# Performance work log

Measured on AMD Instinct MI355X. Metric: run time of the kernel, lower is better.

The kernel has to match this reference:

```python
import jax, jax.numpy as jnp
import numpy as np

BS, X_DIM, KEY_DIM, N_KEYS, TOPK = 16384, 4096, 512, 4096, 16


def setup_inputs() -> dict:
    key = jax.random.key(0)
    k_x, k_keys, k_w, k_b = jax.random.split(key, 4)
    bound = 1.0 / np.sqrt(X_DIM)  # torch Linear default init range
    return {
        "x": jax.random.normal(k_x, (BS, X_DIM), dtype=jnp.float32),
        "keys": jax.random.normal(k_keys, (N_KEYS, KEY_DIM), dtype=jnp.float32),
        "W": jax.random.uniform(k_w, (KEY_DIM, X_DIM), dtype=jnp.float32, minval=-bound, maxval=bound),
        "b": jax.random.uniform(k_b, (KEY_DIM,), dtype=jnp.float32, minval=-bound, maxval=bound),
        "topk": TOPK,
    }


def reference(x, keys, W, b, topk):
    # query = projection(x): [bs, key_dim]
    query = jnp.einsum("bx,kx->bk", x, W) + b
    # scores = query @ keys^T: [bs, n_keys]
    scores = jnp.einsum("bd,nd->bn", query, keys)
    real_topk = min(keys.shape[0], topk)
    topk_scores, topk_idx = jax.lax.top_k(scores, real_topk)  # [bs, k]
    bs = scores.shape[0]
    rows = jnp.arange(bs)[:, None]
    # scatter topk scores into a zero tensor, then softmax over the full row
    gates = jnp.zeros_like(scores).at[rows, topk_idx].set(topk_scores)
    gates = jax.nn.softmax(gates, axis=1)
    return (gates, scores)
```

## Files before the change

### kernel.cpp

```cpp
#include <hip/hip_runtime.h>
#include <stdint.h>

#define BS_T   16384
#define XDIM   4096
#define KDIM   512
#define NKEYS  4096
#define KTOP   16

typedef _Float16 half8  __attribute__((ext_vector_type(8)));
typedef float    floatx4 __attribute__((ext_vector_type(4)));

__device__ static inline void gload_lds16(const void* g, void* l) {
  __builtin_amdgcn_global_load_lds(
      (const __attribute__((address_space(1))) uint32_t*)(uintptr_t)g,
      (__attribute__((address_space(3))) uint32_t*)(uint32_t)(uintptr_t)l,
      16, 0, 0);
}

#define FULL_BAR() do { __builtin_amdgcn_sched_barrier(0); \
                        __builtin_amdgcn_s_barrier(); \
                        __builtin_amdgcn_sched_barrier(0); } while (0)

__global__ __launch_bounds__(256) void cvt_f32_f16_v(const float* __restrict__ in,
                                                     _Float16* __restrict__ out, int n8) {
  int stride = gridDim.x * 256;
  for (int i = blockIdx.x * 256 + threadIdx.x; i < n8; i += stride) {
    float4 v0 = ((const float4*)in)[2 * i];
    float4 v1 = ((const float4*)in)[2 * i + 1];
    half8 h = { (_Float16)v0.x, (_Float16)v0.y, (_Float16)v0.z, (_Float16)v0.w,
                (_Float16)v1.x, (_Float16)v1.y, (_Float16)v1.z, (_Float16)v1.w };
    ((half8*)out)[i] = h;
  }
}

__global__ __launch_bounds__(512, 1)
void gemm1_pipe(const float* __restrict__ X, const _Float16* __restrict__ Wh,
                const float* __restrict__ bias, _Float16* __restrict__ Q) {
  __shared__ __align__(16) _Float16 ldsA[2][64 * 64];
  __shared__ __align__(16) _Float16 ldsB[2][512 * 64];

  const int tid  = threadIdx.x;
  const int lane = tid & 63;
  const int wid  = tid >> 6;
  const int rowBase = blockIdx.x * 64;
  const int wc  = wid * 64;
  const int l15 = lane & 15;
  const int q4  = lane >> 4;
  const int sub   = lane >> 3;
  const int gslot = (lane & 7) ^ sub;

  const int arow  = tid >> 3;
  const int aslot = tid & 7;
  const float* aSrcT = X + (size_t)(rowBase + arow) * XDIM + aslot * 8;
  const int aoff = arow * 128 + ((aslot * 16) ^ ((arow & 7) << 4));
  const _Float16* const bSrc = Wh + (size_t)(wc + sub) * XDIM + gslot * 8;

  auto stageB = [&](int kt, int buf) {
    char* bd = (char*)&ldsB[buf][0] + wid * 8192;
    #pragma unroll
    for (int i = 0; i < 8; ++i)
      gload_lds16(bSrc + (size_t)i * 8 * XDIM + kt, bd + i * 1024);
  };
  auto writeA = [&](int buf, float4 v0, float4 v1) {
    half8 h = { (_Float16)v0.x, (_Float16)v0.y, (_Float16)v0.z, (_Float16)v0.w,
                (_Float16)v1.x, (_Float16)v1.y, (_Float16)v1.z, (_Float16)v1.w };
    *(half8*)((char*)&ldsA[buf][0] + aoff) = h;
  };
  auto ld8 = [&](const char* base, int row, int s) {
    return *(const half8*)(base + row * 128 + ((s * 16) ^ ((row & 7) << 4)));
  };

  floatx4 acc[4][4];
  #pragma unroll
  for (int m = 0; m < 4; ++m)
    #pragma unroll
    for (int n = 0; n < 4; ++n)
      acc[m][n] = (floatx4)0.0f;

  float4 p0  = *(const float4*)(aSrcT);
  float4 p1  = *(const float4*)(aSrcT + 4);
  float4 aw0 = *(const float4*)(aSrcT + 64);
  float4 aw1 = *(const float4*)(aSrcT + 68);
  stageB(0, 0);
  stageB(64, 1);
  writeA(0, p0, p1);
  asm volatile("s_waitcnt lgkmcnt(0)" ::: "memory");
  asm volatile("s_waitcnt vmcnt(8)" ::: "memory");
  FULL_BAR();

  #pragma unroll 2
  for (int t = 0; t < 64; ++t) {
    const int cu = t & 1;
    const char* bA = (const char*)&ldsA[cu][0];
    const char* bB = (const char*)&ldsB[cu][0];

    half8 a[4][2], b[4][2];
    #pragma unroll
    for (int m = 0; m < 4; ++m)
      #pragma unroll
      for (int kk = 0; kk < 2; ++kk)
        a[m][kk] = ld8(bA, m * 16 + l15, kk * 4 + q4);
    #pragma unroll
    for (int n = 0; n < 4; ++n)
      #pragma unroll
      for (int kk = 0; kk < 2; ++kk)
        b[n][kk] = ld8(bB, wc + n * 16 + l15, kk * 4 + q4);
    float4 nl0, nl1;
    if (t < 62) {
      nl0 = *(const float4*)(aSrcT + (t + 2) * 64);
      nl1 = *(const float4*)(aSrcT + (t + 2) * 64 + 4);
    }
    asm volatile("s_waitcnt lgkmcnt(0)" ::: "memory");
    __builtin_amdgcn_sched_barrier(0);
    if (t < 62) stageB((t + 2) * 64, cu);
    __builtin_amdgcn_sched_barrier(0);

    __builtin_amdgcn_s_setprio(1);
    #pragma unroll
    for (int m = 0; m < 4; ++m)
      #pragma unroll
      for (int n = 0; n < 4; ++n)
        #pragma unroll
        for (int kk = 0; kk < 2; ++kk)
          acc[m][n] = __builtin_amdgcn_mfma_f32_16x16x32_f16(a[m][kk], b[n][kk], acc[m][n], 0, 0, 0);
    __builtin_amdgcn_s_setprio(0);

    if (t < 63) writeA(cu ^ 1, aw0, aw1);
    asm volatile("s_waitcnt lgkmcnt(0)" ::: "memory");
    __builtin_amdgcn_sched_barrier(0);
    if (t < 62)       asm volatile("s_waitcnt vmcnt(10)" ::: "memory");
    else if (t == 62) asm volatile("s_waitcnt vmcnt(0)"  ::: "memory");
    FULL_BAR();
    aw0 = nl0; aw1 = nl1;
  }

  #pragma unroll
  for (int m = 0; m < 4; ++m) {
    #pragma unroll
    for (int n = 0; n < 4; ++n) {
      int col = wc + n * 16 + l15;
      float bv = bias[col];
      #pragma unroll
      for (int r = 0; r < 4; ++r) {
        int row = rowBase + m * 16 + q4 * 4 + r;
        Q[(size_t)row * KDIM + col] = (_Float16)(acc[m][n][r] + bv);
      }
    }
  }
}

__global__ __launch_bounds__(512, 2)
void gemm2_pipe(const _Float16* __restrict__ Aq, const _Float16* __restrict__ Bk,
                float* __restrict__ outp) {
  __shared__ __align__(16) _Float16 ldsA[2][256 * 64];
  __shared__ __align__(16) _Float16 ldsB[2][256 * 64];

  const int tid  = threadIdx.x;
  const int lane = tid & 63;
  const int wid  = tid >> 6;
  const int cpx  = gridDim.x >> 3;
  const int bid  = (blockIdx.x & 7) * cpx + (blockIdx.x >> 3);
  const int nCol = NKEYS / 256;
  const int rowBase = (bid / nCol) * 256;
  const int colBase = (bid % nCol) * 256;
  const int wm = wid >> 2;
  const int wn = wid & 3;
  const int l15 = lane & 15;
  const int q4  = lane >> 4;
  const int sub   = lane >> 3;
  const int gslot = (lane & 7) ^ sub;

  const _Float16* aSrc = Aq + (size_t)rowBase * KDIM;
  const _Float16* bSrc = Bk + (size_t)colBase * KDIM;

  auto stageHalf = [&](const _Float16* src, char* ldsbase, int kt, int h) {
    #pragma unroll
    for (int j = 0; j < 2; ++j) {
      int g = h * 16 + wid * 2 + j;
      gload_lds16(src + (size_t)(g * 8 + sub) * KDIM + kt + gslot * 8,
                  ldsbase + g * 1024);
    }
  };
  auto ld8 = [&](const char* base, int row, int s) {
    return *(const half8*)(base + row * 128 + ((s * 16) ^ ((row & 7) << 4)));
  };

  floatx4 acc[8][4];
  #pragma unroll
  for (int m = 0; m < 8; ++m)
    #pragma unroll
    for (int n = 0; n < 4; ++n)
      acc[m][n] = (floatx4)0.0f;

  stageHalf(aSrc, (char*)ldsA[0], 0, 0);
  stageHalf(aSrc, (char*)ldsA[0], 0, 1);
  stageHalf(bSrc, (char*)ldsB[0], 0, 0);
  stageHalf(bSrc, (char*)ldsB[0], 0, 1);
  stageHalf(aSrc, (char*)ldsA[1], 64, 0);
  stageHalf(aSrc, (char*)ldsA[1], 64, 1);
  stageHalf(bSrc, (char*)ldsB[1], 64, 0);
  stageHalf(bSrc, (char*)ldsB[1], 64, 1);
  asm volatile("s_waitcnt vmcnt(8)" ::: "memory");
  FULL_BAR();

  for (int t = 0; t < 8; ++t) {
    const char* bA = (const char*)ldsA[t & 1];
    const char* bB = (const char*)ldsB[t & 1];
    char* sA = (char*)ldsA[t & 1];
    char* sB = (char*)ldsB[t & 1];
    const int ktn = (t + 2) * 64;
    const bool st = (t < 6);

    half8 a[4][2], b[4][2];

    #pragma unroll
    for (int m = 0; m < 4; ++m)
      #pragma unroll
      for (int kk = 0; kk < 2; ++kk)
        a[m][kk] = ld8(bA, wm * 128 + m * 16 + l15, kk * 4 + q4);
    #pragma unroll
    for (int n = 0; n < 4; ++n)
      #pragma unroll
      for (int kk = 0; kk < 2; ++kk)
        b[n][kk] = ld8(bB, wn * 64 + n * 16 + l15, kk * 4 + q4);
    FULL_BAR();
    asm volatile("s_waitcnt lgkmcnt(0)" ::: "memory");
    __builtin_amdgcn_sched_barrier(0);
    __builtin_amdgcn_s_setprio(1);
    #pragma unroll
    for (int m = 0; m < 4; ++m)
      #pragma unroll
      for (int n = 0; n < 2; ++n)
        #pragma unroll
        for (int kk = 0; kk < 2; ++kk)
          acc[m][n] = __builtin_amdgcn_mfma_f32_16x16x32_f16(a[m][kk], b[n][kk], acc[m][n], 0, 0, 0);
    __builtin_amdgcn_s_setprio(0);
    FULL_BAR();

    if (st) stageHalf(bSrc, sB, ktn, 0);
    __builtin_amdgcn_sched_barrier(0);
    __builtin_amdgcn_s_setprio(1);
    #pragma unroll
    for (int m = 0; m < 4; ++m)
      #pragma unroll
      for (int n = 2; n < 4; ++n)
        #pragma unroll
        for (int kk = 0; kk < 2; ++kk)
          acc[m][n] = __builtin_amdgcn_mfma_f32_16x16x32_f16(a[m][kk], b[n][kk], acc[m][n], 0, 0, 0);
    __builtin_amdgcn_s_setprio(0);
    FULL_BAR();

    #pragma unroll
    for (int m = 0; m < 4; ++m)
      #pragma unroll
      for (int kk = 0; kk < 2; ++kk)
        a[m][kk] = ld8(bA, wm * 128 + (m + 4) * 16 + l15, kk * 4 + q4);
    if (st) stageHalf(bSrc, sB, ktn, 1);
    FULL_BAR();
    asm volatile("s_waitcnt lgkmcnt(0)" ::: "memory");
    __builtin_amdgcn_sched_barrier(0);
    __builtin_amdgcn_s_setprio(1);
    #pragma unroll
    for (int m = 0; m < 4; ++m)
      #pragma unroll
      for (int n = 0; n < 2; ++n)
        #pragma unroll
        for (int kk = 0; kk < 2; ++kk)
          acc[m + 4][n] = __builtin_amdgcn_mfma_f32_16x16x32_f16(a[m][kk], b[n][kk], acc[m + 4][n], 0, 0, 0);
    __builtin_amdgcn_s_setprio(0);
    FULL_BAR();

    if (st) { stageHalf(aSrc, sA, ktn, 0); stageHalf(aSrc, sA, ktn, 1); }
    __builtin_amdgcn_sched_barrier(0);
    __builtin_amdgcn_s_setprio(1);
    #pragma unroll
    for (int m = 0; m < 4; ++m)
      #pragma unroll
      for (int n = 2; n < 4; ++n)
        #pragma unroll
        for (int kk = 0; kk < 2; ++kk)
          acc[m + 4][n] = __builtin_amdgcn_mfma_f32_16x16x32_f16(a[m][kk], b[n][kk], acc[m + 4][n], 0, 0, 0);
    __builtin_amdgcn_s_setprio(0);
    __builtin_amdgcn_sched_barrier(0);
    if (t < 6)      asm volatile("s_waitcnt vmcnt(8)" ::: "memory");
    else if (t == 6) asm volatile("s_waitcnt vmcnt(0)" ::: "memory");
    FULL_BAR();
  }

  #pragma unroll
  for (int m = 0; m < 8; ++m) {
    #pragma unroll
    for (int n = 0; n < 4; ++n) {
      int col = colBase + wn * 64 + n * 16 + l15;
      #pragma unroll
      for (int r = 0; r < 4; ++r) {
        int row = rowBase + wm * 128 + m * 16 + q4 * 4 + r;
        outp[(size_t)row * NKEYS + col] = acc[m][n][r];
      }
    }
  }
}

__global__ __launch_bounds__(256) void topk_gates_kernel(const float* __restrict__ scores,
                                                         float* __restrict__ gates) {
  __shared__ uint32_t hist[4096];
  __shared__ uint32_t sA[256];
  __shared__ uint32_t av[16], ai[16];
  __shared__ uint32_t sk[KTOP], si[KTOP];
  __shared__ uint32_t cntA, cntC;
  __shared__ int s_p; __shared__ uint32_t s_above;
  __shared__ float gk[KTOP]; __shared__ float s_gother;

  const int tid  = threadIdx.x;
  const int lane = tid & 63;
  const int w    = tid >> 6;
  const float* srow = scores + (size_t)blockIdx.x * NKEYS;

  uint4 z4 = {0, 0, 0, 0};
  #pragma unroll
  for (int i = 0; i < 4; ++i) ((uint4*)hist)[tid + 256 * i] = z4;
  if (tid == 0) { cntA = 0; cntC = 0; }

  uint32_t key[16];
  const int base = (w << 10) + (lane << 4);
  {
    const float4* p4 = (const float4*)(srow + base);
    #pragma unroll
    for (int i = 0; i < 4; ++i) {
      float4 t = p4[i];
      float tv[4] = { t.x, t.y, t.z, t.w };
      #pragma unroll
      for (int c = 0; c < 4; ++c) {
        uint32_t u = __float_as_uint(tv[c]);
        key[i * 4 + c] = u ^ (uint32_t)(((int32_t)u >> 31) | 0x80000000);
      }
    }
  }
  __syncthreads();

  #pragma unroll
  for (int j = 0; j < 16; ++j) atomicAdd(&hist[key[j] >> 20], 1u);
  __syncthreads();

  uint32_t h[16];
  #pragma unroll
  for (int i = 0; i < 16; ++i) h[i] = hist[tid * 16 + i];
  uint32_t sfx[17]; sfx[16] = 0;
  #pragma unroll
  for (int i = 15; i >= 0; --i) sfx[i] = sfx[i + 1] + h[i];
  sA[tid] = sfx[0];
  __syncthreads();
  uint32_t s = sfx[0];
  #pragma unroll
  for (int off = 1; off < 256; off <<= 1) {
    uint32_t add = (tid + off < 256) ? sA[tid + off] : 0;
    __syncthreads();
    s += add; sA[tid] = s;
    __syncthreads();
  }
  const uint32_t exclHi = s - sfx[0];

  #pragma unroll
  for (int i = 0; i < 16; ++i) {
    uint32_t cg = exclHi + sfx[i + 1];
    if (cg < KTOP && cg + h[i] >= KTOP) { s_p = tid * 16 + i; s_above = cg; }
  }
  __syncthreads();
  const uint32_t p = (uint32_t)s_p;
  const uint32_t above = s_above;
  const uint32_t need = KTOP - above;

  uint32_t* ck = hist;
  uint32_t* ci = hist + 2048;
  #pragma unroll
  for (int j = 0; j < 16; ++j) {
    uint32_t b = key[j] >> 20;
    if (b >= p) {
      uint32_t idx = (uint32_t)(base + j);
      if (b > p) { uint32_t pos = atomicAdd(&cntA, 1u); av[pos] = key[j]; ai[pos] = idx; }
      else       { uint32_t pos = atomicAdd(&cntC, 1u); if (pos < 2048u) { ck[pos] = key[j]; ci[pos] = idx; } }
    }
  }
  __syncthreads();

  const uint32_t nA = cntA;
  if (tid < nA) { sk[tid] = av[tid]; si[tid] = ai[tid]; }

  if (w == 0) {
    const uint32_t nC = min(cntC, 2048u);
    for (uint32_t k = 0; k < need; ++k) {
      uint32_t bk = 0, bi = 0xFFFFFFFFu, bp = 0;
      for (uint32_t c = lane; c < nC; c += 64) {
        uint32_t kk = ck[c], ii = ci[c];
        if (kk > bk || (kk == bk && ii < bi)) { bk = kk; bi = ii; bp = c; }
      }
      #pragma unroll
      for (int off = 32; off >= 1; off >>= 1) {
        uint32_t ok = __shfl_down(bk, off);
        uint32_t oi = __shfl_down(bi, off);
        uint32_t op = __shfl_down(bp, off);
        if (ok > bk || (ok == bk && oi < bi)) { bk = ok; bi = oi; bp = op; }
      }
      bp = __shfl(bp, 0);
      if (lane == 0) { ck[bp] = 0; sk[nA + k] = bk; si[nA + k] = bi; }
    }
  }
  __syncthreads();

  if (tid == 0) {
    float f[KTOP]; float mx = 0.f;
    #pragma unroll
    for (int k = 0; k < KTOP; ++k) {
      uint32_t kk = sk[k];
      float fv = (kk & 0x80000000u) ? __uint_as_float(kk ^ 0x80000000u)
                                    : __uint_as_float(~kk);
      f[k] = fv; mx = fmaxf(mx, fv);
    }
    float eo = __expf(-mx);
    float Z = (float)(NKEYS - KTOP) * eo;
    float e[KTOP];
    #pragma unroll
    for (int k = 0; k < KTOP; ++k) { e[k] = __expf(f[k] - mx); Z += e[k]; }
    float inv = 1.f / Z;
    #pragma unroll
    for (int k = 0; k < KTOP; ++k) gk[k] = e[k] * inv;
    s_gother = eo * inv;
  }
  __syncthreads();

  float go = s_gother;
  float4 g4 = { go, go, go, go };
  float* grow = gates + (size_t)blockIdx.x * NKEYS;
  #pragma unroll
  for (int j = 0; j < 4; ++j) ((float4*)grow)[j * 256 + tid] = g4;
  __syncthreads();
  if (tid < KTOP) grow[si[tid]] = gk[tid];
}

extern "C" void kernel_launch(void* const* d_in, const int* in_sizes, int n_in,
                              void* d_out, int out_size, void* d_ws, size_t ws_size,
                              hipStream_t stream) {
  const float* x    = (const float*)d_in[0];
  const float* keys = (const float*)d_in[1];
  const float* W    = (const float*)d_in[2];
  const float* bias = (const float*)d_in[3];
  (void)in_sizes; (void)n_in; (void)out_size; (void)ws_size;

  float* gates  = (float*)d_out;
  float* scores = (float*)d_out + (size_t)BS_T * NKEYS;

  _Float16* W_h = (_Float16*)d_ws;
  _Float16* k_h = W_h + (size_t)KDIM * XDIM;
  _Float16* q_h = k_h + (size_t)NKEYS * KDIM;

  cvt_f32_f16_v<<<dim3(1024), dim3(256), 0, stream>>>(W, W_h, KDIM * XDIM / 8);
  cvt_f32_f16_v<<<dim3(1024), dim3(256), 0, stream>>>(keys, k_h, NKEYS * KDIM / 8);

  gemm1_pipe<<<dim3(BS_T / 64), dim3(512), 0, stream>>>(x, W_h, bias, q_h);

  gemm2_pipe<<<dim3((BS_T / 256) * (NKEYS / 256)), dim3(512), 0, stream>>>(
      q_h, k_h, scores);

  topk_gates_kernel<<<dim3(BS_T), dim3(256), 0, stream>>>(scores, gates);
}
```

Measured before the change: 344.9 us.

## Split gemm1 into 256-thread column-half blocks with XCD-aware block remap

```diff
diff --git a/kernel.cpp b/kernel.cpp
--- a/kernel.cpp
+++ b/kernel.cpp
@@ -17,6 +17,7 @@
       16, 0, 0);
 }
 
+#define SBAR() __builtin_amdgcn_sched_barrier(0)
 #define FULL_BAR() do { __builtin_amdgcn_sched_barrier(0); \
                         __builtin_amdgcn_s_barrier(); \
                         __builtin_amdgcn_sched_barrier(0); } while (0)
@@ -33,16 +34,19 @@
   }
 }
 
-__global__ __launch_bounds__(512, 1)
+__global__ __launch_bounds__(256, 2)
 void gemm1_pipe(const float* __restrict__ X, const _Float16* __restrict__ Wh,
                 const float* __restrict__ bias, _Float16* __restrict__ Q) {
   __shared__ __align__(16) _Float16 ldsA[2][64 * 64];
-  __shared__ __align__(16) _Float16 ldsB[2][512 * 64];
+  __shared__ __align__(16) _Float16 ldsB[2][256 * 64];
 
   const int tid  = threadIdx.x;
   const int lane = tid & 63;
   const int wid  = tid >> 6;
-  const int rowBase = blockIdx.x * 64;
+  const int cpx  = gridDim.x >> 3;
+  const int bid  = (blockIdx.x & 7) * cpx + (blockIdx.x >> 3);
+  const int rowBase = (bid >> 1) * 64;
+  const int colBase = (bid & 1) * 256;
   const int wc  = wid * 64;
   const int l15 = lane & 15;
   const int q4  = lane >> 4;
@@ -51,9 +55,10 @@
 
   const int arow  = tid >> 3;
   const int aslot = tid & 7;
-  const float* aSrcT = X + (size_t)(rowBase + arow) * XDIM + aslot * 8;
+  const float* aSrc0 = X + (size_t)(rowBase + arow) * XDIM + aslot * 8;
+  const float* aSrc1 = aSrc0 + (size_t)32 * XDIM;
   const int aoff = arow * 128 + ((aslot * 16) ^ ((arow & 7) << 4));
-  const _Float16* const bSrc = Wh + (size_t)(wc + sub) * XDIM + gslot * 8;
+  const _Float16* const bSrc = Wh + (size_t)(colBase + wc + sub) * XDIM + gslot * 8;
 
   auto stageB = [&](int kt, int buf) {
     char* bd = (char*)&ldsB[buf][0] + wid * 8192;
@@ -61,10 +66,13 @@
     for (int i = 0; i < 8; ++i)
       gload_lds16(bSrc + (size_t)i * 8 * XDIM + kt, bd + i * 1024);
   };
-  auto writeA = [&](int buf, float4 v0, float4 v1) {
-    half8 h = { (_Float16)v0.x, (_Float16)v0.y, (_Float16)v0.z, (_Float16)v0.w,
-                (_Float16)v1.x, (_Float16)v1.y, (_Float16)v1.z, (_Float16)v1.w };
-    *(half8*)((char*)&ldsA[buf][0] + aoff) = h;
+  auto writeA = [&](int buf, float4 v00, float4 v01, float4 v10, float4 v11) {
+    half8 h0 = { (_Float16)v00.x, (_Float16)v00.y, (_Float16)v00.z, (_Float16)v00.w,
+                 (_Float16)v01.x, (_Float16)v01.y, (_Float16)v01.z, (_Float16)v01.w };
+    half8 h1 = { (_Float16)v10.x, (_Float16)v10.y, (_Float16)v10.z, (_Float16)v10.w,
+                 (_Float16)v11.x, (_Float16)v11.y, (_Float16)v11.z, (_Float16)v11.w };
+    *(half8*)((char*)&ldsA[buf][0] + aoff) = h0;
+    *(half8*)((char*)&ldsA[buf][0] + aoff + 4096) = h1;
   };
   auto ld8 = [&](const char* base, int row, int s) {
     return *(const half8*)(base + row * 128 + ((s * 16) ^ ((row & 7) << 4)));
@@ -77,13 +85,21 @@
     for (int n = 0; n < 4; ++n)
       acc[m][n] = (floatx4)0.0f;
 
-  float4 p0  = *(const float4*)(aSrcT);
-  float4 p1  = *(const float4*)(aSrcT + 4);
-  float4 aw0 = *(const float4*)(aSrcT + 64);
-  float4 aw1 = *(const float4*)(aSrcT + 68);
+  float4 p00 = *(const float4*)(aSrc0);
+  float4 p01 = *(const float4*)(aSrc0 + 4);
+  float4 p10 = *(const float4*)(aSrc1);
+  float4 p11 = *(const float4*)(aSrc1 + 4);
+  SBAR();
+  float4 aw00 = *(const float4*)(aSrc0 + 64);
+  float4 aw01 = *(const float4*)(aSrc0 + 68);
+  float4 aw10 = *(const float4*)(aSrc1 + 64);
+  float4 aw11 = *(const float4*)(aSrc1 + 68);
+  SBAR();
   stageB(0, 0);
+  SBAR();
   stageB(64, 1);
-  writeA(0, p0, p1);
+  SBAR();
+  writeA(0, p00, p01, p10, p11);
   asm volatile("s_waitcnt lgkmcnt(0)" ::: "memory");
   asm volatile("s_waitcnt vmcnt(8)" ::: "memory");
   FULL_BAR();
@@ -105,15 +121,19 @@
       #pragma unroll
       for (int kk = 0; kk < 2; ++kk)
         b[n][kk] = ld8(bB, wc + n * 16 + l15, kk * 4 + q4);
-    float4 nl0, nl1;
+    float4 nl00, nl01, nl10, nl11;
     if (t < 62) {
-      nl0 = *(const float4*)(aSrcT + (t + 2) * 64);
-      nl1 = *(const float4*)(aSrcT + (t + 2) * 64 + 4);
-    }
+      const int ktn = (t + 2) * 64;
+      nl00 = *(const float4*)(aSrc0 + ktn);
+      nl01 = *(const float4*)(aSrc0 + ktn + 4);
+      nl10 = *(const float4*)(aSrc1 + ktn);
+      nl11 = *(const float4*)(aSrc1 + ktn + 4);
+    }
+    SBAR();
     asm volatile("s_waitcnt lgkmcnt(0)" ::: "memory");
-    __builtin_amdgcn_sched_barrier(0);
+    SBAR();
     if (t < 62) stageB((t + 2) * 64, cu);
-    __builtin_amdgcn_sched_barrier(0);
+    SBAR();
 
     __builtin_amdgcn_s_setprio(1);
     #pragma unroll
@@ -125,20 +145,20 @@
           acc[m][n] = __builtin_amdgcn_mfma_f32_16x16x32_f16(a[m][kk], b[n][kk], acc[m][n], 0, 0, 0);
     __builtin_amdgcn_s_setprio(0);
 
-    if (t < 63) writeA(cu ^ 1, aw0, aw1);
+    if (t < 63) writeA(cu ^ 1, aw00, aw01, aw10, aw11);
     asm volatile("s_waitcnt lgkmcnt(0)" ::: "memory");
-    __builtin_amdgcn_sched_barrier(0);
-    if (t < 62)       asm volatile("s_waitcnt vmcnt(10)" ::: "memory");
+    SBAR();
+    if (t < 62)       asm volatile("s_waitcnt vmcnt(12)" ::: "memory");
     else if (t == 62) asm volatile("s_waitcnt vmcnt(0)"  ::: "memory");
     FULL_BAR();
-    aw0 = nl0; aw1 = nl1;
+    aw00 = nl00; aw01 = nl01; aw10 = nl10; aw11 = nl11;
   }
 
   #pragma unroll
   for (int m = 0; m < 4; ++m) {
     #pragma unroll
     for (int n = 0; n < 4; ++n) {
-      int col = wc + n * 16 + l15;
+      int col = colBase + wc + n * 16 + l15;
       float bv = bias[col];
       #pragma unroll
       for (int r = 0; r < 4; ++r) {
@@ -456,7 +476,7 @@
   cvt_f32_f16_v<<<dim3(1024), dim3(256), 0, stream>>>(W, W_h, KDIM * XDIM / 8);
   cvt_f32_f16_v<<<dim3(1024), dim3(256), 0, stream>>>(keys, k_h, NKEYS * KDIM / 8);
 
-  gemm1_pipe<<<dim3(BS_T / 64), dim3(512), 0, stream>>>(x, W_h, bias, q_h);
+  gemm1_pipe<<<dim3((BS_T / 64) * 2), dim3(256), 0, stream>>>(x, W_h, bias, q_h);
 
   gemm2_pipe<<<dim3((BS_T / 256) * (NKEYS / 256)), dim3(512), 0, stream>>>(
       q_h, k_h, scores);
```

After: 348.0 us. Within noise of the previous version (+0.9%).

## Restructure projection GEMM pipeline with 256-wide A chunks and per-wave B buffers

Applied to the files above, without the earlier changes.

```diff
diff --git a/kernel.cpp b/kernel.cpp
--- a/kernel.cpp
+++ b/kernel.cpp
@@ -17,6 +17,8 @@
       16, 0, 0);
 }
 
+#define SBAR() __builtin_amdgcn_sched_barrier(0)
+#define LGKM0() asm volatile("s_waitcnt lgkmcnt(0)" ::: "memory")
 #define FULL_BAR() do { __builtin_amdgcn_sched_barrier(0); \
                         __builtin_amdgcn_s_barrier(); \
                         __builtin_amdgcn_sched_barrier(0); } while (0)
@@ -36,8 +38,8 @@
 __global__ __launch_bounds__(512, 1)
 void gemm1_pipe(const float* __restrict__ X, const _Float16* __restrict__ Wh,
                 const float* __restrict__ bias, _Float16* __restrict__ Q) {
-  __shared__ __align__(16) _Float16 ldsA[2][64 * 64];
-  __shared__ __align__(16) _Float16 ldsB[2][512 * 64];
+  __shared__ __align__(16) _Float16 ldsA[2][64 * 256];
+  __shared__ __align__(16) _Float16 ldsB[512 * 64];
 
   const int tid  = threadIdx.x;
   const int lane = tid & 63;
@@ -49,25 +51,29 @@
   const int sub   = lane >> 3;
   const int gslot = (lane & 7) ^ sub;
 
-  const int arow  = tid >> 3;
-  const int aslot = tid & 7;
-  const float* aSrcT = X + (size_t)(rowBase + arow) * XDIM + aslot * 8;
-  const int aoff = arow * 128 + ((aslot * 16) ^ ((arow & 7) << 4));
+  const int arow = tid >> 3;
+  const int s    = tid & 7;
+  const float* aSrc = X + (size_t)(rowBase + arow) * XDIM + s * 32;
+  const int au    = (s >> 1) * 8192;
+  const int abyte = arow * 128;
+  const int aswz  = (arow & 7) << 4;
+
   const _Float16* const bSrc = Wh + (size_t)(wc + sub) * XDIM + gslot * 8;
-
-  auto stageB = [&](int kt, int buf) {
-    char* bd = (char*)&ldsB[buf][0] + wid * 8192;
+  char* const bDst = (char*)ldsB + wid * 8192;
+
+  auto stageB = [&](int kt) {
     #pragma unroll
     for (int i = 0; i < 8; ++i)
-      gload_lds16(bSrc + (size_t)i * 8 * XDIM + kt, bd + i * 1024);
-  };
-  auto writeA = [&](int buf, float4 v0, float4 v1) {
+      gload_lds16(bSrc + (size_t)i * 8 * XDIM + kt, bDst + i * 1024);
+  };
+  auto wrA = [&](char* base, int k, float4 v0, float4 v1) {
     half8 h = { (_Float16)v0.x, (_Float16)v0.y, (_Float16)v0.z, (_Float16)v0.w,
                 (_Float16)v1.x, (_Float16)v1.y, (_Float16)v1.z, (_Float16)v1.w };
-    *(half8*)((char*)&ldsA[buf][0] + aoff) = h;
-  };
-  auto ld8 = [&](const char* base, int row, int s) {
-    return *(const half8*)(base + row * 128 + ((s * 16) ^ ((row & 7) << 4)));
+    const int w = (s & 1) * 4 + k;
+    *(half8*)(base + au + abyte + ((w * 16) ^ aswz)) = h;
+  };
+  auto ld8 = [&](const char* base, int row, int w) {
+    return *(const half8*)(base + row * 128 + ((w * 16) ^ ((row & 7) << 4)));
   };
 
   floatx4 acc[4][4];
@@ -77,44 +83,20 @@
     for (int n = 0; n < 4; ++n)
       acc[m][n] = (floatx4)0.0f;
 
-  float4 p0  = *(const float4*)(aSrcT);
-  float4 p1  = *(const float4*)(aSrcT + 4);
-  float4 aw0 = *(const float4*)(aSrcT + 64);
-  float4 aw1 = *(const float4*)(aSrcT + 68);
-  stageB(0, 0);
-  stageB(64, 1);
-  writeA(0, p0, p1);
-  asm volatile("s_waitcnt lgkmcnt(0)" ::: "memory");
-  asm volatile("s_waitcnt vmcnt(8)" ::: "memory");
-  FULL_BAR();
-
-  #pragma unroll 2
-  for (int t = 0; t < 64; ++t) {
-    const int cu = t & 1;
-    const char* bA = (const char*)&ldsA[cu][0];
-    const char* bB = (const char*)&ldsB[cu][0];
-
-    half8 a[4][2], b[4][2];
+  half8 a[4][2], b[4][2];
+  auto readFrags = [&](const char* aB) {
     #pragma unroll
     for (int m = 0; m < 4; ++m)
       #pragma unroll
       for (int kk = 0; kk < 2; ++kk)
-        a[m][kk] = ld8(bA, m * 16 + l15, kk * 4 + q4);
+        a[m][kk] = ld8(aB, m * 16 + l15, kk * 4 + q4);
     #pragma unroll
     for (int n = 0; n < 4; ++n)
       #pragma unroll
       for (int kk = 0; kk < 2; ++kk)
-        b[n][kk] = ld8(bB, wc + n * 16 + l15, kk * 4 + q4);
-    float4 nl0, nl1;
-    if (t < 62) {
-      nl0 = *(const float4*)(aSrcT + (t + 2) * 64);
-      nl1 = *(const float4*)(aSrcT + (t + 2) * 64 + 4);
-    }
-    asm volatile("s_waitcnt lgkmcnt(0)" ::: "memory");
-    __builtin_amdgcn_sched_barrier(0);
-    if (t < 62) stageB((t + 2) * 64, cu);
-    __builtin_amdgcn_sched_barrier(0);
-
+        b[n][kk] = ld8((const char*)ldsB, wc + n * 16 + l15, kk * 4 + q4);
+  };
+  auto mfma32 = [&]() {
     __builtin_amdgcn_s_setprio(1);
     #pragma unroll
     for (int m = 0; m < 4; ++m)
@@ -124,14 +106,93 @@
         for (int kk = 0; kk < 2; ++kk)
           acc[m][n] = __builtin_amdgcn_mfma_f32_16x16x32_f16(a[m][kk], b[n][kk], acc[m][n], 0, 0, 0);
     __builtin_amdgcn_s_setprio(0);
-
-    if (t < 63) writeA(cu ^ 1, aw0, aw1);
-    asm volatile("s_waitcnt lgkmcnt(0)" ::: "memory");
-    __builtin_amdgcn_sched_barrier(0);
-    if (t < 62)       asm volatile("s_waitcnt vmcnt(10)" ::: "memory");
-    else if (t == 62) asm volatile("s_waitcnt vmcnt(0)"  ::: "memory");
-    FULL_BAR();
-    aw0 = nl0; aw1 = nl1;
+  };
+
+  float4 P0a, P0b, P1a, P1b, P2a, P2b, P3a, P3b, N0a, N0b;
+
+  {
+    float4 C0 = *(const float4*)(aSrc + 0),  C1 = *(const float4*)(aSrc + 4);
+    float4 C2 = *(const float4*)(aSrc + 8),  C3 = *(const float4*)(aSrc + 12);
+    float4 C4 = *(const float4*)(aSrc + 16), C5 = *(const float4*)(aSrc + 20);
+    float4 C6 = *(const float4*)(aSrc + 24), C7 = *(const float4*)(aSrc + 28);
+    SBAR();
+    stageB(0);
+    SBAR();
+    P0a = *(const float4*)(aSrc + 256);
+    P0b = *(const float4*)(aSrc + 260);
+    SBAR();
+    char* w0 = (char*)&ldsA[0][0];
+    wrA(w0, 0, C0, C1); wrA(w0, 1, C2, C3);
+    wrA(w0, 2, C4, C5); wrA(w0, 3, C6, C7);
+    LGKM0();
+    asm volatile("s_waitcnt vmcnt(2)" ::: "memory");
+    FULL_BAR();
+  }
+
+  for (int c = 0; c < 16; ++c) {
+    const char* aB = (const char*)&ldsA[c & 1][0];
+    const int t0 = c * 4;
+    const int cb = (c + 1) * 256;
+
+    readFrags(aB);
+    LGKM0(); SBAR();
+    stageB((t0 + 1) * 64);
+    SBAR();
+    if (c < 15) { P1a = *(const float4*)(aSrc + cb + 8);
+                  P1b = *(const float4*)(aSrc + cb + 12); }
+    SBAR();
+    mfma32();
+    SBAR();
+    if (c < 15) asm volatile("s_waitcnt vmcnt(2)" ::: "memory");
+    else        asm volatile("s_waitcnt vmcnt(0)" ::: "memory");
+    SBAR();
+
+    readFrags(aB + 8192);
+    LGKM0(); SBAR();
+    stageB((t0 + 2) * 64);
+    SBAR();
+    if (c < 15) { P2a = *(const float4*)(aSrc + cb + 16);
+                  P2b = *(const float4*)(aSrc + cb + 20); }
+    SBAR();
+    mfma32();
+    SBAR();
+    if (c < 15) asm volatile("s_waitcnt vmcnt(2)" ::: "memory");
+    else        asm volatile("s_waitcnt vmcnt(0)" ::: "memory");
+    SBAR();
+
+    readFrags(aB + 2 * 8192);
+    LGKM0(); SBAR();
+    stageB((t0 + 3) * 64);
+    SBAR();
+    if (c < 15) { P3a = *(const float4*)(aSrc + cb + 24);
+                  P3b = *(const float4*)(aSrc + cb + 28); }
+    SBAR();
+    mfma32();
+    SBAR();
+    if (c < 15) asm volatile("s_waitcnt vmcnt(2)" ::: "memory");
+    else        asm volatile("s_waitcnt vmcnt(0)" ::: "memory");
+    SBAR();
+
+    readFrags(aB + 3 * 8192);
+    LGKM0(); SBAR();
+    if (c < 15) stageB((t0 + 4) * 64);
+    SBAR();
+    if (c < 14) { N0a = *(const float4*)(aSrc + (c + 2) * 256);
+                  N0b = *(const float4*)(aSrc + (c + 2) * 256 + 4); }
+    SBAR();
+    if (c < 15) {
+      char* wB = (char*)&ldsA[(c + 1) & 1][0];
+      wrA(wB, 0, P0a, P0b); wrA(wB, 1, P1a, P1b);
+      wrA(wB, 2, P2a, P2b); wrA(wB, 3, P3a, P3b);
+    }
+    SBAR();
+    mfma32();
+    SBAR();
+    if (c < 14)      asm volatile("s_waitcnt vmcnt(2)" ::: "memory");
+    else if (c < 15) asm volatile("s_waitcnt vmcnt(0)" ::: "memory");
+    LGKM0();
+    if (c < 15) FULL_BAR();
+    P0a = N0a; P0b = N0b;
   }
 
   #pragma unroll
```

After: 369.3 us. +7.1%, slower.

## Restructure gemm1 A-tile staging to load two K-steps per chunk

Applied to the files above, without the earlier changes.

```diff
diff --git a/kernel.cpp b/kernel.cpp
--- a/kernel.cpp
+++ b/kernel.cpp
@@ -17,6 +17,8 @@
       16, 0, 0);
 }
 
+#define SBAR() __builtin_amdgcn_sched_barrier(0)
+#define LGKM0() asm volatile("s_waitcnt lgkmcnt(0)" ::: "memory")
 #define FULL_BAR() do { __builtin_amdgcn_sched_barrier(0); \
                         __builtin_amdgcn_s_barrier(); \
                         __builtin_amdgcn_sched_barrier(0); } while (0)
@@ -36,7 +38,7 @@
 __global__ __launch_bounds__(512, 1)
 void gemm1_pipe(const float* __restrict__ X, const _Float16* __restrict__ Wh,
                 const float* __restrict__ bias, _Float16* __restrict__ Q) {
-  __shared__ __align__(16) _Float16 ldsA[2][64 * 64];
+  __shared__ __align__(16) _Float16 ldsA[64 * 128];
   __shared__ __align__(16) _Float16 ldsB[2][512 * 64];
 
   const int tid  = threadIdx.x;
@@ -49,10 +51,14 @@
   const int sub   = lane >> 3;
   const int gslot = (lane & 7) ^ sub;
 
-  const int arow  = tid >> 3;
-  const int aslot = tid & 7;
-  const float* aSrcT = X + (size_t)(rowBase + arow) * XDIM + aslot * 8;
-  const int aoff = arow * 128 + ((aslot * 16) ^ ((arow & 7) << 4));
+  const int arow = tid >> 3;
+  const int s    = tid & 7;
+  const float* aSrc = X + (size_t)(rowBase + arow) * XDIM + s * 16;
+  const int au    = (s >> 2) * 8192;
+  const int abyte = arow * 128;
+  const int aswz  = (arow & 7) << 4;
+  const int w0    = (s & 3) * 2;
+
   const _Float16* const bSrc = Wh + (size_t)(wc + sub) * XDIM + gslot * 8;
 
   auto stageB = [&](int kt, int buf) {
@@ -61,13 +67,16 @@
     for (int i = 0; i < 8; ++i)
       gload_lds16(bSrc + (size_t)i * 8 * XDIM + kt, bd + i * 1024);
   };
-  auto writeA = [&](int buf, float4 v0, float4 v1) {
-    half8 h = { (_Float16)v0.x, (_Float16)v0.y, (_Float16)v0.z, (_Float16)v0.w,
-                (_Float16)v1.x, (_Float16)v1.y, (_Float16)v1.z, (_Float16)v1.w };
-    *(half8*)((char*)&ldsA[buf][0] + aoff) = h;
-  };
-  auto ld8 = [&](const char* base, int row, int s) {
-    return *(const half8*)(base + row * 128 + ((s * 16) ^ ((row & 7) << 4)));
+  auto writeA = [&](float4 v0, float4 v1, float4 v2, float4 v3) {
+    half8 h0 = { (_Float16)v0.x, (_Float16)v0.y, (_Float16)v0.z, (_Float16)v0.w,
+                 (_Float16)v1.x, (_Float16)v1.y, (_Float16)v1.z, (_Float16)v1.w };
+    half8 h1 = { (_Float16)v2.x, (_Float16)v2.y, (_Float16)v2.z, (_Float16)v2.w,
+                 (_Float16)v3.x, (_Float16)v3.y, (_Float16)v3.z, (_Float16)v3.w };
+    *(half8*)((char*)ldsA + au + abyte + ((w0 * 16) ^ aswz)) = h0;
+    *(half8*)((char*)ldsA + au + abyte + (((w0 + 1) * 16) ^ aswz)) = h1;
+  };
+  auto ld8 = [&](const char* base, int row, int sl) {
+    return *(const half8*)(base + row * 128 + ((sl * 16) ^ ((row & 7) << 4)));
   };
 
   floatx4 acc[4][4];
@@ -77,44 +86,20 @@
     for (int n = 0; n < 4; ++n)
       acc[m][n] = (floatx4)0.0f;
 
-  float4 p0  = *(const float4*)(aSrcT);
-  float4 p1  = *(const float4*)(aSrcT + 4);
-  float4 aw0 = *(const float4*)(aSrcT + 64);
-  float4 aw1 = *(const float4*)(aSrcT + 68);
-  stageB(0, 0);
-  stageB(64, 1);
-  writeA(0, p0, p1);
-  asm volatile("s_waitcnt lgkmcnt(0)" ::: "memory");
-  asm volatile("s_waitcnt vmcnt(8)" ::: "memory");
-  FULL_BAR();
-
-  #pragma unroll 2
-  for (int t = 0; t < 64; ++t) {
-    const int cu = t & 1;
-    const char* bA = (const char*)&ldsA[cu][0];
-    const char* bB = (const char*)&ldsB[cu][0];
-
-    half8 a[4][2], b[4][2];
+  half8 a[4][2], b[4][2];
+  auto readFrags = [&](const char* aB, const char* bB) {
     #pragma unroll
     for (int m = 0; m < 4; ++m)
       #pragma unroll
       for (int kk = 0; kk < 2; ++kk)
-        a[m][kk] = ld8(bA, m * 16 + l15, kk * 4 + q4);
+        a[m][kk] = ld8(aB, m * 16 + l15, kk * 4 + q4);
     #pragma unroll
     for (int n = 0; n < 4; ++n)
       #pragma unroll
       for (int kk = 0; kk < 2; ++kk)
         b[n][kk] = ld8(bB, wc + n * 16 + l15, kk * 4 + q4);
-    float4 nl0, nl1;
-    if (t < 62) {
-      nl0 = *(const float4*)(aSrcT + (t + 2) * 64);
-      nl1 = *(const float4*)(aSrcT + (t + 2) * 64 + 4);
-    }
-    asm volatile("s_waitcnt lgkmcnt(0)" ::: "memory");
-    __builtin_amdgcn_sched_barrier(0);
-    if (t < 62) stageB((t + 2) * 64, cu);
-    __builtin_amdgcn_sched_barrier(0);
-
+  };
+  auto mfma32 = [&]() {
     __builtin_amdgcn_s_setprio(1);
     #pragma unroll
     for (int m = 0; m < 4; ++m)
@@ -124,14 +109,56 @@
         for (int kk = 0; kk < 2; ++kk)
           acc[m][n] = __builtin_amdgcn_mfma_f32_16x16x32_f16(a[m][kk], b[n][kk], acc[m][n], 0, 0, 0);
     __builtin_amdgcn_s_setprio(0);
-
-    if (t < 63) writeA(cu ^ 1, aw0, aw1);
-    asm volatile("s_waitcnt lgkmcnt(0)" ::: "memory");
-    __builtin_amdgcn_sched_barrier(0);
-    if (t < 62)       asm volatile("s_waitcnt vmcnt(10)" ::: "memory");
-    else if (t == 62) asm volatile("s_waitcnt vmcnt(0)"  ::: "memory");
-    FULL_BAR();
-    aw0 = nl0; aw1 = nl1;
+  };
+
+  {
+    float4 C0 = *(const float4*)(aSrc + 0), C1 = *(const float4*)(aSrc + 4);
+    float4 C2 = *(const float4*)(aSrc + 8), C3 = *(const float4*)(aSrc + 12);
+    SBAR();
+    stageB(0, 0);
+    SBAR();
+    stageB(64, 1);
+    SBAR();
+    writeA(C0, C1, C2, C3);
+    LGKM0();
+    asm volatile("s_waitcnt vmcnt(8)" ::: "memory");
+    FULL_BAR();
+  }
+
+  float4 N0, N1, N2, N3;
+
+  for (int c = 0; c < 32; ++c) {
+    if (c > 0) {
+      writeA(N0, N1, N2, N3);
+      LGKM0();
+      FULL_BAR();
+    }
+    readFrags((const char*)ldsA, (const char*)&ldsB[0][0]);
+    LGKM0(); SBAR();
+    if (c < 31) stageB((2 * c + 2) * 64, 0);
+    SBAR();
+    if (c < 31) {
+      const float* nsrc = aSrc + (c + 1) * 128;
+      N0 = *(const float4*)(nsrc + 0); N1 = *(const float4*)(nsrc + 4);
+      N2 = *(const float4*)(nsrc + 8); N3 = *(const float4*)(nsrc + 12);
+    }
+    SBAR();
+    mfma32();
+    SBAR();
+    if (c < 31) asm volatile("s_waitcnt vmcnt(12)" ::: "memory");
+    else        asm volatile("s_waitcnt vmcnt(0)"  ::: "memory");
+    FULL_BAR();
+
+    readFrags((const char*)ldsA + 8192, (const char*)&ldsB[1][0]);
+    LGKM0(); SBAR();
+    if (c < 31) stageB((2 * c + 3) * 64, 1);
+    SBAR();
+    mfma32();
+    SBAR();
+    if (c < 31) {
+      asm volatile("s_waitcnt vmcnt(12)" ::: "memory");
+      FULL_BAR();
+    }
   }
 
   #pragma unroll
```

Measured after the change: 347.7 us. No clear change (+0.8%).
